# Optimization experiments

Measured on AMD Instinct MI355X. Metric: run time of the kernel, lower is better.

The kernel has to match this reference:

```python
import jax, jax.numpy as jnp
import numpy as np

B, NPG, C = 16, 4096, 256          # graphs, nodes per graph per type, feat dim
N = B * NPG                        # nodes per type
E = N * 16                         # edges per edge type (avg degree 16)
RATIO = 0.25
K = int(np.ceil(RATIO * NPG))      # top-k nodes per graph per type


def setup_inputs() -> dict:
    key = jax.random.key(0)
    ks = jax.random.split(key, 16)
    s = 1.0 / np.sqrt(C)
    inp = {
        "x_inst": jax.random.normal(ks[0], (N, C), jnp.float32),
        "x_data": jax.random.normal(ks[1], (N, C), jnp.float32),
        "w_kqv_inst": jax.random.normal(ks[2], (C, 3), jnp.float32) * s,
        "b_kqv_inst": jnp.zeros((3,), jnp.float32),
        "w_kqv_data": jax.random.normal(ks[3], (C, 3), jnp.float32) * s,
        "b_kqv_data": jnp.zeros((3,), jnp.float32),
        "w_out_inst": jax.random.normal(ks[4], (1, 1), jnp.float32),
        "b_out_inst": jnp.zeros((1,), jnp.float32),
        "w_out_data": jax.random.normal(ks[5], (1, 1), jnp.float32),
        "b_out_data": jnp.zeros((1,), jnp.float32),
        "krel_w": jax.random.normal(ks[6], (3,), jnp.float32),
        "krel_b": jnp.zeros((3,), jnp.float32),
        "vrel_w": jax.random.normal(ks[7], (3,), jnp.float32),
        "vrel_b": jnp.zeros((3,), jnp.float32),
        "p_rel": jnp.ones((3,), jnp.float32),
        "ei_i2d": jax.random.randint(ks[8], (2, E), 0, N, jnp.int32),
        "ei_d2i": jax.random.randint(ks[9], (2, E), 0, N, jnp.int32),
        "ei_i2i": jax.random.randint(ks[10], (2, E), 0, N, jnp.int32),
        "batch_inst": jnp.repeat(jnp.arange(B, dtype=jnp.int32), NPG),
        "batch_data": jnp.repeat(jnp.arange(B, dtype=jnp.int32), NPG),
    }
    return inp


def _hgt_scores(x_inst, x_data, w_kqv_inst, b_kqv_inst, w_kqv_data, b_kqv_data,
                w_out_inst, b_out_inst, w_out_data, b_out_data,
                krel_w, krel_b, vrel_w, vrel_b, p_rel,
                ei_i2d, ei_d2i, ei_i2i):
    # HGTConv with out_channels=1, heads=1 -> H=1, D=1 (k,q,v scalar per node)
    kqv_i = x_inst @ w_kqv_inst + b_kqv_inst   # [N,3]
    kqv_d = x_data @ w_kqv_data + b_kqv_data
    k_i, q_i, v_i = kqv_i[:, 0], kqv_i[:, 1], kqv_i[:, 2]
    k_d, q_d, v_d = kqv_d[:, 0], kqv_d[:, 1], kqv_d[:, 2]
    # dst offsets follow node-type order: inst=0, data=N
    q_glob = jnp.concatenate([q_i, q_d])       # [2N]
    Ntot = 2 * N

    def edge_terms(k_src, v_src, ei, t, dst_off):
        s, d = ei[0], ei[1]
        ke = k_src[s] * krel_w[t] + krel_b[t]  # per-relation 1x1 k_rel
        ve = v_src[s] * vrel_w[t] + vrel_b[t]  # per-relation 1x1 v_rel
        dg = d + dst_off
        logit = q_glob[dg] * ke * p_rel[t]     # (q_i*k_j).sum * p_rel / sqrt(D=1)
        return logit, ve, dg

    l0, v0, d0 = edge_terms(k_i, v_i, ei_i2d, 0, N)  # inst->data (dst=data)
    l1, v1, d1 = edge_terms(k_d, v_d, ei_d2i, 1, 0)  # data->inst (dst=inst)
    l2, v2, d2 = edge_terms(k_i, v_i, ei_i2i, 2, 0)  # inst->inst (dst=inst)
    logits = jnp.concatenate([l0, l1, l2])
    vals = jnp.concatenate([v0, v1, v2])
    dst = jnp.concatenate([d0, d1, d2])

    # segment softmax over incoming edges of each destination node
    m = jax.ops.segment_max(logits, dst, num_segments=Ntot)
    m = jnp.where(jnp.isfinite(m), m, 0.0)
    ex = jnp.exp(logits - m[dst])
    den = jax.ops.segment_sum(ex, dst, num_segments=Ntot)
    alpha = ex / den[dst]
    a = jax.ops.segment_sum(alpha * vals, dst, num_segments=Ntot)  # [2N]

    # out_lin (1->1) per node type; skip inactive (1 != 256); GELU (exact)
    s_i = jax.nn.gelu(a[:N, None] * w_out_inst[0, 0] + b_out_inst, approximate=False)
    s_d = jax.nn.gelu(a[N:, None] * w_out_data[0, 0] + b_out_data, approximate=False)
    return s_i, s_d  # [N,1] each


def _pool(x, score):
    # per-graph top-k on score, gate by tanh(score), mean over selected
    sv = score[:, 0].reshape(B, NPG)
    xv = x.reshape(B, NPG, -1)
    topv, topi = jax.lax.top_k(sv, K)                      # [B,K]
    xs = jnp.take_along_axis(xv, topi[:, :, None], axis=1)  # [B,K,C]
    return (xs * jnp.tanh(topv)[:, :, None]).mean(axis=1)   # [B,C]


def reference(x_inst, x_data, w_kqv_inst, b_kqv_inst, w_kqv_data, b_kqv_data,
              w_out_inst, b_out_inst, w_out_data, b_out_data,
              krel_w, krel_b, vrel_w, vrel_b, p_rel,
              ei_i2d, ei_d2i, ei_i2i, batch_inst, batch_data):
    # batch_* are uniform [B x NPG] blocks; pooling uses reshape equivalently.
    s_i, s_d = _hgt_scores(x_inst, x_data, w_kqv_inst, b_kqv_inst,
                           w_kqv_data, b_kqv_data, w_out_inst, b_out_inst,
                           w_out_data, b_out_data, krel_w, krel_b,
                           vrel_w, vrel_b, p_rel, ei_i2d, ei_d2i, ei_i2i)
    return jnp.concatenate([_pool(x_inst, s_i), _pool(x_data, s_d)], axis=-1)  # [B, 2C]
```

## Files before the change

### kernel.cpp

```cpp
#include <hip/hip_runtime.h>
#include <math.h>

constexpr int BB   = 16;
constexpr int NPGc = 4096;
constexpr int Cc   = 256;
constexpr int Nc   = BB * NPGc;
constexpr int Ec   = Nc * 16;
constexpr int Kc   = 1024;
constexpr int NBUK = 1024;
constexpr int BUKW = 128;
constexpr int CHUNK = 16384;
constexpr int NCHUNK = (3 * Ec) / CHUNK;

__device__ __forceinline__ unsigned fkey(float f) {
    int b = __float_as_int(f);
    unsigned u = (unsigned)b;
    return (b < 0) ? ~u : (u | 0x80000000u);
}
__device__ __forceinline__ float inv_fkey(unsigned u) {
    unsigned b = (u & 0x80000000u) ? (u ^ 0x80000000u) : ~u;
    return __int_as_float((int)b);
}

__global__ __launch_bounds__(256) void kqv_kernel(
    const float* __restrict__ x_inst, const float* __restrict__ x_data,
    const float* __restrict__ w_inst, const float* __restrict__ b_inst,
    const float* __restrict__ w_data, const float* __restrict__ b_data,
    float2* __restrict__ kv_i, float2* __restrict__ kv_d,
    float* __restrict__ q_glob)
{
    int tid  = threadIdx.x;
    int wave = tid >> 6, lane = tid & 63;
    int grp  = lane >> 4, l = lane & 15;
    int g    = blockIdx.x * 16 + wave * 4 + grp;
    int row0 = g * 2;
    int side = (row0 >= Nc) ? 1 : 0;
    int node0 = row0 - side * Nc;
    const float* x  = side ? x_data : x_inst;
    const float* w  = side ? w_data : w_inst;
    const float* bp = side ? b_data : b_inst;
    float2* kv = side ? kv_d : kv_i;

    float wr[48];
#pragma unroll
    for (int it = 0; it < 4; ++it) {
        const float4* wv = (const float4*)(w + (it * 64 + l * 4) * 3);
        float4 f0 = wv[0], f1 = wv[1], f2 = wv[2];
        wr[it*12+0]=f0.x; wr[it*12+1]=f0.y; wr[it*12+2]=f0.z; wr[it*12+3]=f0.w;
        wr[it*12+4]=f1.x; wr[it*12+5]=f1.y; wr[it*12+6]=f1.z; wr[it*12+7]=f1.w;
        wr[it*12+8]=f2.x; wr[it*12+9]=f2.y; wr[it*12+10]=f2.z; wr[it*12+11]=f2.w;
    }
    float b0 = bp[0], b1 = bp[1], b2 = bp[2];

    const float4* rp = (const float4*)(x + (size_t)node0 * Cc);
    float4 xv[2][4];
#pragma unroll
    for (int r = 0; r < 2; ++r)
#pragma unroll
        for (int it = 0; it < 4; ++it)
            xv[r][it] = rp[r * 64 + it * 16 + l];

#pragma unroll
    for (int r = 0; r < 2; ++r) {
        float kk = 0.f, qq = 0.f, vv = 0.f;
#pragma unroll
        for (int it = 0; it < 4; ++it) {
            float xs[4] = {xv[r][it].x, xv[r][it].y, xv[r][it].z, xv[r][it].w};
#pragma unroll
            for (int u = 0; u < 4; ++u) {
                float xd = xs[u];
                kk = fmaf(xd, wr[it * 12 + u * 3 + 0], kk);
                qq = fmaf(xd, wr[it * 12 + u * 3 + 1], qq);
                vv = fmaf(xd, wr[it * 12 + u * 3 + 2], vv);
            }
        }
#pragma unroll
        for (int off = 8; off; off >>= 1) {
            kk += __shfl_xor(kk, off, 64);
            qq += __shfl_xor(qq, off, 64);
            vv += __shfl_xor(vv, off, 64);
        }
        if (l == 0) {
            int node = node0 + r;
            kv[node] = make_float2(kk + b0, vv + b2);
            q_glob[side * Nc + node] = qq + b1;
        }
    }
}

__global__ __launch_bounds__(256) void count_kernel(
    const int* __restrict__ ei0, const int* __restrict__ ei1,
    const int* __restrict__ ei2, unsigned* __restrict__ bucket_cnt)
{
    __shared__ unsigned hist[NBUK];
    int tid = threadIdx.x;
    for (int j = tid; j < NBUK; j += 256) hist[j] = 0;
    __syncthreads();
    unsigned base = blockIdx.x * (unsigned)CHUNK;
    int t = (int)(base >> 20);
    unsigned i0 = base & (unsigned)(Ec - 1);
    const int* ei = (t == 0) ? ei0 : (t == 1) ? ei1 : ei2;
    int off = (t == 0) ? Nc : 0;
    const int4* dv = (const int4*)(ei + Ec + i0);
#pragma unroll 4
    for (int j = 0; j < CHUNK / 1024; ++j) {
        int4 d4 = dv[j * 256 + tid];
        atomicAdd(&hist[(unsigned)(d4.x + off) >> 7], 1u);
        atomicAdd(&hist[(unsigned)(d4.y + off) >> 7], 1u);
        atomicAdd(&hist[(unsigned)(d4.z + off) >> 7], 1u);
        atomicAdd(&hist[(unsigned)(d4.w + off) >> 7], 1u);
    }
    __syncthreads();
    for (int j = tid; j < NBUK; j += 256)
        if (hist[j]) atomicAdd(&bucket_cnt[j], hist[j]);
}

__global__ __launch_bounds__(1024) void scan_kernel(
    const unsigned* __restrict__ bucket_cnt,
    unsigned* __restrict__ bucket_base, unsigned* __restrict__ bucket_fill)
{
    __shared__ unsigned s[NBUK];
    int t = threadIdx.x;
    unsigned mine = bucket_cnt[t];
    s[t] = mine;
    __syncthreads();
    for (int off = 1; off < NBUK; off <<= 1) {
        unsigned v = (t >= off) ? s[t - off] : 0u;
        __syncthreads();
        s[t] += v;
        __syncthreads();
    }
    unsigned ex = s[t] - mine;
    bucket_base[t] = ex;
    bucket_fill[t] = ex;
    if (t == NBUK - 1) bucket_base[NBUK] = s[t];
}

__global__ __launch_bounds__(256) void fill_kernel(
    const int* __restrict__ ei0, const int* __restrict__ ei1,
    const int* __restrict__ ei2, unsigned* __restrict__ bucket_fill,
    unsigned* __restrict__ sorted)
{
    __shared__ unsigned hist[NBUK];
    __shared__ unsigned res[NBUK];
    int tid = threadIdx.x;
    for (int j = tid; j < NBUK; j += 256) hist[j] = 0;
    __syncthreads();
    unsigned base = blockIdx.x * (unsigned)CHUNK;
    int t = (int)(base >> 20);
    unsigned i0 = base & (unsigned)(Ec - 1);
    const int* ei = (t == 0) ? ei0 : (t == 1) ? ei1 : ei2;
    int off = (t == 0) ? Nc : 0;
    const int4* dv = (const int4*)(ei + Ec + i0);
    const int4* sv = (const int4*)(ei + i0);
#pragma unroll 4
    for (int j = 0; j < CHUNK / 1024; ++j) {
        int4 d4 = dv[j * 256 + tid];
        atomicAdd(&hist[(unsigned)(d4.x + off) >> 7], 1u);
        atomicAdd(&hist[(unsigned)(d4.y + off) >> 7], 1u);
        atomicAdd(&hist[(unsigned)(d4.z + off) >> 7], 1u);
        atomicAdd(&hist[(unsigned)(d4.w + off) >> 7], 1u);
    }
    __syncthreads();
    for (int j = tid; j < NBUK; j += 256) {
        unsigned h = hist[j];
        res[j] = h ? atomicAdd(&bucket_fill[j], h) : 0u;
        hist[j] = 0;
    }
    __syncthreads();
#pragma unroll 4
    for (int j = 0; j < CHUNK / 1024; ++j) {
        int4 d4 = dv[j * 256 + tid];
        int4 s4 = sv[j * 256 + tid];
        int dd[4] = {d4.x, d4.y, d4.z, d4.w};
        int ss[4] = {s4.x, s4.y, s4.z, s4.w};
#pragma unroll
        for (int u = 0; u < 4; ++u) {
            int dg  = dd[u] + off;
            int bkt = dg >> 7;
            unsigned local = atomicAdd(&hist[bkt], 1u);
            sorted[res[bkt] + local] =
                (unsigned)ss[u] | ((unsigned)t << 16) | ((unsigned)(dg & 127) << 18);
        }
    }
}

__global__ __launch_bounds__(256) void bucket_accum_kernel(
    const unsigned* __restrict__ bucket_base, const unsigned* __restrict__ sorted,
    const float* __restrict__ krel_w, const float* __restrict__ krel_b,
    const float* __restrict__ vrel_w, const float* __restrict__ vrel_b,
    const float* __restrict__ p_rel,
    const float2* __restrict__ kv_i, const float2* __restrict__ kv_d,
    const float* __restrict__ q_glob,
    float* __restrict__ den, float* __restrict__ num)
{
    __shared__ float den_l[BUKW];
    __shared__ float num_l[BUKW];
    __shared__ float q_l[BUKW];
    int tid = threadIdx.x;
    int b   = blockIdx.x;
    if (tid < BUKW) {
        den_l[tid] = 0.0f;
        num_l[tid] = 0.0f;
        q_l[tid]   = q_glob[b * BUKW + tid];
    }
    float kw0 = krel_w[0], kw1 = krel_w[1], kw2 = krel_w[2];
    float kb0 = krel_b[0], kb1 = krel_b[1], kb2 = krel_b[2];
    float vw0 = vrel_w[0], vw1 = vrel_w[1], vw2 = vrel_w[2];
    float vb0 = vrel_b[0], vb1 = vrel_b[1], vb2 = vrel_b[2];
    float pr0 = p_rel[0],  pr1 = p_rel[1],  pr2 = p_rel[2];
    unsigned beg = bucket_base[b], end = bucket_base[b + 1];
    __syncthreads();

    for (unsigned e = beg + tid; e < end; e += 256) {
        unsigned r = sorted[e];
        int s    = (int)(r & 0xFFFFu);
        int t    = (int)((r >> 16) & 3u);
        int low7 = (int)((r >> 18) & 127u);
        float2 kvv = (t == 1) ? kv_d[s] : kv_i[s];
        float kwt = (t == 0) ? kw0 : (t == 1) ? kw1 : kw2;
        float kbt = (t == 0) ? kb0 : (t == 1) ? kb1 : kb2;
        float vwt = (t == 0) ? vw0 : (t == 1) ? vw1 : vw2;
        float vbt = (t == 0) ? vb0 : (t == 1) ? vb1 : vb2;
        float prt = (t == 0) ? pr0 : (t == 1) ? pr1 : pr2;
        float ke = fmaf(kvv.x, kwt, kbt);
        float ve = fmaf(kvv.y, vwt, vbt);
        float logit = q_l[low7] * ke * prt;
        float ex = __expf(fminf(logit, 80.0f));
        __hip_atomic_fetch_add(&den_l[low7], ex, __ATOMIC_RELAXED,
                               __HIP_MEMORY_SCOPE_WORKGROUP);
        __hip_atomic_fetch_add(&num_l[low7], ex * ve, __ATOMIC_RELAXED,
                               __HIP_MEMORY_SCOPE_WORKGROUP);
    }
    __syncthreads();
    if (tid < BUKW) {
        den[b * BUKW + tid] = den_l[tid];
        num[b * BUKW + tid] = num_l[tid];
    }
}

__global__ __launch_bounds__(1024) void select_kernel(
    const float* __restrict__ den, const float* __restrict__ num,
    const float* __restrict__ w_out_inst, const float* __restrict__ b_out_inst,
    const float* __restrict__ w_out_data, const float* __restrict__ b_out_data,
    int* __restrict__ sel_idx, float* __restrict__ sel_w)
{
    __shared__ unsigned keys[NPGc];
    __shared__ unsigned hist[2048];
    __shared__ unsigned wsum[16];
    __shared__ unsigned short cand[NPGc];
    __shared__ unsigned sh_bin1, sh_rem1, sh_bin2, sh_rem2, sh_cnt, sh_nc;

    int tid  = threadIdx.x;
    int seg  = blockIdx.x;
    int side = seg >> 4;
    int b    = seg & 15;
    float wo = side ? w_out_data[0] : w_out_inst[0];
    float bo = side ? b_out_data[0] : b_out_inst[0];
    int base_node = side * Nc + b * NPGc;
    int base_sel  = seg * Kc;

    unsigned myk[4]; int myj[4];
#pragma unroll
    for (int p = 0; p < 4; ++p) {
        int j = p * 1024 + tid;
        float dn = den[base_node + j];
        float a  = (dn > 0.0f) ? num[base_node + j] / dn : 0.0f;
        float z  = fmaf(a, wo, bo);
        float s  = 0.5f * z * (1.0f + erff(z * 0.70710678f));
        unsigned k32 = fkey(s);
        keys[j] = k32; myk[p] = k32; myj[p] = j;
    }
    if (tid == 0) { sh_cnt = 0; sh_nc = 0; }
    hist[tid] = 0; hist[tid + 1024] = 0;
    __syncthreads();

#pragma unroll
    for (int p = 0; p < 4; ++p) atomicAdd(&hist[myk[p] >> 21], 1u);
    __syncthreads();
    {
        unsigned g0 = hist[2047 - 2 * tid];
        unsigned g1 = hist[2046 - 2 * tid];
        unsigned x = g0 + g1;
        int lane = tid & 63;
#pragma unroll
        for (int off = 1; off < 64; off <<= 1) {
            unsigned y = __shfl_up(x, off, 64);
            if (lane >= off) x += y;
        }
        if (lane == 63) wsum[tid >> 6] = x;
        __syncthreads();
        if (tid < 16) {
            unsigned v = wsum[tid];
#pragma unroll
            for (int off = 1; off < 16; off <<= 1) {
                unsigned y = __shfl_up(v, off, 64);
                if (tid >= off) v += y;
            }
            wsum[tid] = v;
        }
        __syncthreads();
        unsigned basew = (tid >= 64) ? wsum[(tid >> 6) - 1] : 0u;
        unsigned incl  = basew + x;
        unsigned incl0 = incl - g1;
        unsigned K = Kc;
        if (incl0 >= K && incl0 - g0 < K) { sh_bin1 = 2047 - 2 * tid; sh_rem1 = K - (incl0 - g0); }
        if (incl  >= K && incl0     < K) { sh_bin1 = 2046 - 2 * tid; sh_rem1 = K - incl0; }
    }
    __syncthreads();
    unsigned bin1 = sh_bin1, rem1 = sh_rem1;
    hist[tid] = 0; hist[tid + 1024] = 0;
    __syncthreads();

#pragma unroll
    for (int p = 0; p < 4; ++p)
        if ((myk[p] >> 21) == bin1)
            atomicAdd(&hist[(myk[p] >> 10) & 2047u], 1u);
    __syncthreads();
    {
        unsigned g0 = hist[2047 - 2 * tid];
        unsigned g1 = hist[2046 - 2 * tid];
        unsigned x = g0 + g1;
        int lane = tid & 63;
#pragma unroll
        for (int off = 1; off < 64; off <<= 1) {
            unsigned y = __shfl_up(x, off, 64);
            if (lane >= off) x += y;
        }
        if (lane == 63) wsum[tid >> 6] = x;
        __syncthreads();
        if (tid < 16) {
            unsigned v = wsum[tid];
#pragma unroll
            for (int off = 1; off < 16; off <<= 1) {
                unsigned y = __shfl_up(v, off, 64);
                if (tid >= off) v += y;
            }
            wsum[tid] = v;
        }
        __syncthreads();
        unsigned basew = (tid >= 64) ? wsum[(tid >> 6) - 1] : 0u;
        unsigned incl  = basew + x;
        unsigned incl0 = incl - g1;
        unsigned K = rem1;
        if (incl0 >= K && incl0 - g0 < K) { sh_bin2 = 2047 - 2 * tid; sh_rem2 = K - (incl0 - g0); }
        if (incl  >= K && incl0     < K) { sh_bin2 = 2046 - 2 * tid; sh_rem2 = K - incl0; }
    }
    __syncthreads();
    unsigned pref22 = (bin1 << 11) | sh_bin2;
    unsigned rem2 = sh_rem2;

#pragma unroll
    for (int p = 0; p < 4; ++p) {
        unsigned top22 = myk[p] >> 10;
        if (top22 > pref22) {
            unsigned pos = atomicAdd(&sh_cnt, 1u);
            sel_idx[base_sel + pos] = myj[p];
            sel_w[base_sel + pos]   = tanhf(inv_fkey(myk[p]));
        } else if (top22 == pref22) {
            unsigned cp = atomicAdd(&sh_nc, 1u);
            cand[cp] = (unsigned short)myj[p];
        }
    }
    __syncthreads();

    unsigned nc = sh_nc;
    for (unsigned c = tid; c < nc; c += 1024) {
        int j = cand[c];
        unsigned k32 = keys[j];
        unsigned rank = 0;
        for (unsigned q = 0; q < nc; ++q) {
            int jq = cand[q];
            unsigned kq = keys[jq];
            rank += (kq > k32 || (kq == k32 && jq < j)) ? 1u : 0u;
        }
        if (rank < rem2) {
            unsigned pos = atomicAdd(&sh_cnt, 1u);
            sel_idx[base_sel + pos] = j;
            sel_w[base_sel + pos]   = tanhf(inv_fkey(k32));
        }
    }
}

__global__ __launch_bounds__(1024) void pool_kernel(
    const float* __restrict__ x_inst, const float* __restrict__ x_data,
    const int* __restrict__ sel_idx, const float* __restrict__ sel_w,
    float* __restrict__ out)
{
    __shared__ int   ridx[64];
    __shared__ float rw[64];
    __shared__ float accs[256];
    int tid   = threadIdx.x;
    int blk   = blockIdx.x;
    int seg   = blk >> 4;
    int chunk = blk & 15;
    int side  = seg >> 4;
    int b     = seg & 15;
    if (tid < 64) {
        ridx[tid] = sel_idx[seg * Kc + chunk * 64 + tid];
        rw[tid]   = sel_w[seg * Kc + chunk * 64 + tid];
    }
    if (tid < 256) accs[tid] = 0.0f;
    __syncthreads();
    const float* x = side ? x_data : x_inst;
    int w = tid >> 6, l = tid & 63;
    float ax = 0.f, ay = 0.f, az = 0.f, aw = 0.f;
#pragma unroll
    for (int r = 0; r < 4; ++r) {
        int   row = ridx[w * 4 + r];
        float wt  = rw[w * 4 + r];
        float4 xv = ((const float4*)(x + ((size_t)(b * NPGc + row)) * Cc))[l];
        ax = fmaf(xv.x, wt, ax); ay = fmaf(xv.y, wt, ay);
        az = fmaf(xv.z, wt, az); aw = fmaf(xv.w, wt, aw);
    }
    atomicAdd(&accs[l * 4 + 0], ax);
    atomicAdd(&accs[l * 4 + 1], ay);
    atomicAdd(&accs[l * 4 + 2], az);
    atomicAdd(&accs[l * 4 + 3], aw);
    __syncthreads();
    if (tid < 256)
        unsafeAtomicAdd(&out[b * 512 + side * 256 + tid], accs[tid] * (1.0f / (float)Kc));
}

extern "C" void kernel_launch(void* const* d_in, const int* in_sizes, int n_in,
                              void* d_out, int out_size, void* d_ws, size_t ws_size,
                              hipStream_t stream) {
    const float* x_inst     = (const float*)d_in[0];
    const float* x_data     = (const float*)d_in[1];
    const float* w_kqv_inst = (const float*)d_in[2];
    const float* b_kqv_inst = (const float*)d_in[3];
    const float* w_kqv_data = (const float*)d_in[4];
    const float* b_kqv_data = (const float*)d_in[5];
    const float* w_out_inst = (const float*)d_in[6];
    const float* b_out_inst = (const float*)d_in[7];
    const float* w_out_data = (const float*)d_in[8];
    const float* b_out_data = (const float*)d_in[9];
    const float* krel_w     = (const float*)d_in[10];
    const float* krel_b     = (const float*)d_in[11];
    const float* vrel_w     = (const float*)d_in[12];
    const float* vrel_b     = (const float*)d_in[13];
    const float* p_rel      = (const float*)d_in[14];
    const int*   ei_i2d     = (const int*)d_in[15];
    const int*   ei_d2i     = (const int*)d_in[16];
    const int*   ei_i2i     = (const int*)d_in[17];
    float* out = (float*)d_out;

    char* ws = (char*)d_ws;
    float2* kv_i   = (float2*)ws;
    float2* kv_d   = kv_i + Nc;
    float*  q_glob = (float*)(kv_d + Nc);
    float*  den    = q_glob + 2 * Nc;
    float*  num    = den + 2 * Nc;
    unsigned* bucket_cnt  = (unsigned*)(num + 2 * Nc);
    unsigned* bucket_base = bucket_cnt + NBUK;
    unsigned* bucket_fill = bucket_base + NBUK + 1;
    int*      sel_idx     = (int*)(bucket_fill + NBUK);
    float*    sel_w       = (float*)(sel_idx + 32 * Kc);
    unsigned* sorted      = (unsigned*)(sel_w + 32 * Kc);

    hipMemsetAsync(bucket_cnt, 0, NBUK * sizeof(unsigned), stream);
    hipMemsetAsync(d_out, 0, (size_t)out_size * sizeof(float), stream);

    count_kernel<<<NCHUNK, 256, 0, stream>>>(ei_i2d, ei_d2i, ei_i2i, bucket_cnt);
    scan_kernel<<<1, NBUK, 0, stream>>>(bucket_cnt, bucket_base, bucket_fill);
    fill_kernel<<<NCHUNK, 256, 0, stream>>>(ei_i2d, ei_d2i, ei_i2i,
                                            bucket_fill, sorted);

    kqv_kernel<<<(2 * Nc) / 32, 256, 0, stream>>>(
        x_inst, x_data, w_kqv_inst, b_kqv_inst, w_kqv_data, b_kqv_data,
        kv_i, kv_d, q_glob);

    bucket_accum_kernel<<<NBUK, 256, 0, stream>>>(
        bucket_base, sorted,
        krel_w, krel_b, vrel_w, vrel_b, p_rel,
        kv_i, kv_d, q_glob, den, num);

    select_kernel<<<32, 1024, 0, stream>>>(
        den, num, w_out_inst, b_out_inst, w_out_data, b_out_data,
        sel_idx, sel_w);

    pool_kernel<<<512, 1024, 0, stream>>>(x_inst, x_data, sel_idx, sel_w, out);
}
```

Baseline: 319.9 us.

## Widen dst buckets, shrink sort chunks, replicate shared accumulators in bucket accumulation

Destination buckets now each cover 256 nodes instead of 128, giving 512 buckets, and the count/fill chunk size is halved so twice as many blocks run. The fill kernel takes write positions with a direct atomic on the per-bucket base instead of a second local counter plus an add. The accumulation kernel runs 512 threads per bucket and splits den/num into two interleaved replicas keyed by thread parity, summing them at the end, to reduce contention on shared atomics. The intent is better parallelism and fewer atomic collisions, at the cost of fewer, larger accumulation blocks and a changed summation order.

```diff
diff --git a/kernel.cpp b/kernel.cpp
--- a/kernel.cpp
+++ b/kernel.cpp
@@ -7,9 +7,9 @@
 constexpr int Nc   = BB * NPGc;
 constexpr int Ec   = Nc * 16;
 constexpr int Kc   = 1024;
-constexpr int NBUK = 1024;
-constexpr int BUKW = 128;
-constexpr int CHUNK = 16384;
+constexpr int NBUK = 512;
+constexpr int BUKW = 256;
+constexpr int CHUNK = 8192;
 constexpr int NCHUNK = (3 * Ec) / CHUNK;
 
 __device__ __forceinline__ unsigned fkey(float f) {
@@ -105,17 +105,17 @@
 #pragma unroll 4
     for (int j = 0; j < CHUNK / 1024; ++j) {
         int4 d4 = dv[j * 256 + tid];
-        atomicAdd(&hist[(unsigned)(d4.x + off) >> 7], 1u);
-        atomicAdd(&hist[(unsigned)(d4.y + off) >> 7], 1u);
-        atomicAdd(&hist[(unsigned)(d4.z + off) >> 7], 1u);
-        atomicAdd(&hist[(unsigned)(d4.w + off) >> 7], 1u);
+        atomicAdd(&hist[(unsigned)(d4.x + off) >> 8], 1u);
+        atomicAdd(&hist[(unsigned)(d4.y + off) >> 8], 1u);
+        atomicAdd(&hist[(unsigned)(d4.z + off) >> 8], 1u);
+        atomicAdd(&hist[(unsigned)(d4.w + off) >> 8], 1u);
     }
     __syncthreads();
     for (int j = tid; j < NBUK; j += 256)
         if (hist[j]) atomicAdd(&bucket_cnt[j], hist[j]);
 }
 
-__global__ __launch_bounds__(1024) void scan_kernel(
+__global__ __launch_bounds__(NBUK) void scan_kernel(
     const unsigned* __restrict__ bucket_cnt,
     unsigned* __restrict__ bucket_base, unsigned* __restrict__ bucket_fill)
 {
@@ -156,16 +156,15 @@
 #pragma unroll 4
     for (int j = 0; j < CHUNK / 1024; ++j) {
         int4 d4 = dv[j * 256 + tid];
-        atomicAdd(&hist[(unsigned)(d4.x + off) >> 7], 1u);
-        atomicAdd(&hist[(unsigned)(d4.y + off) >> 7], 1u);
-        atomicAdd(&hist[(unsigned)(d4.z + off) >> 7], 1u);
-        atomicAdd(&hist[(unsigned)(d4.w + off) >> 7], 1u);
+        atomicAdd(&hist[(unsigned)(d4.x + off) >> 8], 1u);
+        atomicAdd(&hist[(unsigned)(d4.y + off) >> 8], 1u);
+        atomicAdd(&hist[(unsigned)(d4.z + off) >> 8], 1u);
+        atomicAdd(&hist[(unsigned)(d4.w + off) >> 8], 1u);
     }
     __syncthreads();
     for (int j = tid; j < NBUK; j += 256) {
         unsigned h = hist[j];
         res[j] = h ? atomicAdd(&bucket_fill[j], h) : 0u;
-        hist[j] = 0;
     }
     __syncthreads();
 #pragma unroll 4
@@ -177,15 +176,15 @@
 #pragma unroll
         for (int u = 0; u < 4; ++u) {
             int dg  = dd[u] + off;
-            int bkt = dg >> 7;
-            unsigned local = atomicAdd(&hist[bkt], 1u);
-            sorted[res[bkt] + local] =
-                (unsigned)ss[u] | ((unsigned)t << 16) | ((unsigned)(dg & 127) << 18);
-        }
-    }
-}
-
-__global__ __launch_bounds__(256) void bucket_accum_kernel(
+            int bkt = dg >> 8;
+            unsigned pos = atomicAdd(&res[bkt], 1u);
+            sorted[pos] =
+                (unsigned)ss[u] | ((unsigned)t << 16) | ((unsigned)(dg & 255) << 18);
+        }
+    }
+}
+
+__global__ __launch_bounds__(512) void bucket_accum_kernel(
     const unsigned* __restrict__ bucket_base, const unsigned* __restrict__ sorted,
     const float* __restrict__ krel_w, const float* __restrict__ krel_b,
     const float* __restrict__ vrel_w, const float* __restrict__ vrel_b,
@@ -194,29 +193,27 @@
     const float* __restrict__ q_glob,
     float* __restrict__ den, float* __restrict__ num)
 {
-    __shared__ float den_l[BUKW];
-    __shared__ float num_l[BUKW];
+    __shared__ float den_l[2 * BUKW];
+    __shared__ float num_l[2 * BUKW];
     __shared__ float q_l[BUKW];
     int tid = threadIdx.x;
     int b   = blockIdx.x;
-    if (tid < BUKW) {
-        den_l[tid] = 0.0f;
-        num_l[tid] = 0.0f;
-        q_l[tid]   = q_glob[b * BUKW + tid];
-    }
+    den_l[tid] = 0.0f; num_l[tid] = 0.0f;
+    if (tid < BUKW) q_l[tid] = q_glob[b * BUKW + tid];
     float kw0 = krel_w[0], kw1 = krel_w[1], kw2 = krel_w[2];
     float kb0 = krel_b[0], kb1 = krel_b[1], kb2 = krel_b[2];
     float vw0 = vrel_w[0], vw1 = vrel_w[1], vw2 = vrel_w[2];
     float vb0 = vrel_b[0], vb1 = vrel_b[1], vb2 = vrel_b[2];
     float pr0 = p_rel[0],  pr1 = p_rel[1],  pr2 = p_rel[2];
     unsigned beg = bucket_base[b], end = bucket_base[b + 1];
-    __syncthreads();
-
-    for (unsigned e = beg + tid; e < end; e += 256) {
+    int rep = tid & 1;
+    __syncthreads();
+
+    for (unsigned e = beg + tid; e < end; e += 512) {
         unsigned r = sorted[e];
         int s    = (int)(r & 0xFFFFu);
         int t    = (int)((r >> 16) & 3u);
-        int low7 = (int)((r >> 18) & 127u);
+        int low8 = (int)((r >> 18) & 255u);
         float2 kvv = (t == 1) ? kv_d[s] : kv_i[s];
         float kwt = (t == 0) ? kw0 : (t == 1) ? kw1 : kw2;
         float kbt = (t == 0) ? kb0 : (t == 1) ? kb1 : kb2;
@@ -225,17 +222,18 @@
         float prt = (t == 0) ? pr0 : (t == 1) ? pr1 : pr2;
         float ke = fmaf(kvv.x, kwt, kbt);
         float ve = fmaf(kvv.y, vwt, vbt);
-        float logit = q_l[low7] * ke * prt;
+        float logit = q_l[low8] * ke * prt;
         float ex = __expf(fminf(logit, 80.0f));
-        __hip_atomic_fetch_add(&den_l[low7], ex, __ATOMIC_RELAXED,
+        int slot = low8 * 2 + rep;
+        __hip_atomic_fetch_add(&den_l[slot], ex, __ATOMIC_RELAXED,
                                __HIP_MEMORY_SCOPE_WORKGROUP);
-        __hip_atomic_fetch_add(&num_l[low7], ex * ve, __ATOMIC_RELAXED,
+        __hip_atomic_fetch_add(&num_l[slot], ex * ve, __ATOMIC_RELAXED,
                                __HIP_MEMORY_SCOPE_WORKGROUP);
     }
     __syncthreads();
     if (tid < BUKW) {
-        den[b * BUKW + tid] = den_l[tid];
-        num[b * BUKW + tid] = num_l[tid];
+        den[b * BUKW + tid] = den_l[tid * 2] + den_l[tid * 2 + 1];
+        num[b * BUKW + tid] = num_l[tid * 2] + num_l[tid * 2 + 1];
     }
 }
 
@@ -470,7 +468,7 @@
         x_inst, x_data, w_kqv_inst, b_kqv_inst, w_kqv_data, b_kqv_data,
         kv_i, kv_d, q_glob);
 
-    bucket_accum_kernel<<<NBUK, 256, 0, stream>>>(
+    bucket_accum_kernel<<<NBUK, 512, 0, stream>>>(
         bucket_base, sorted,
         krel_w, krel_b, vrel_w, vrel_b, p_rel,
         kv_i, kv_d, q_glob, den, num);
```

New measurement: 307.3 us. 3.9% less time.
